# Performance work log

Measured on AMD Instinct MI355X. Metric: run time of the kernel, lower is better.

Reference implementation:

```python
import jax, jax.numpy as jnp
import numpy as np
from jax import lax

SPIKE_RATE = 100.0
TIME_STEPS = 100
ADAPT_FACTOR = 0.95
REFRACTORY = 2.0
N_NEURONS = 256


def setup_inputs() -> dict:
    key = jax.random.key(0)
    x = jax.random.normal(jax.random.fold_in(key, 1), (32, 64), dtype=jnp.float32)
    centers = jnp.linspace(-1.0, 1.0, N_NEURONS).astype(jnp.float32)
    widths = jnp.full((N_NEURONS,), 0.2, dtype=jnp.float32)
    adaptation_state = jnp.ones((N_NEURONS,), dtype=jnp.float32)
    refractory_state = jnp.zeros((N_NEURONS,), dtype=jnp.float32)
    return {
        "x": x,
        "centers": centers,
        "widths": widths,
        "adaptation_state": adaptation_state,
        "refractory_state": refractory_state,
        "seed": 0,
    }


def reference(x, centers, widths, adaptation_state, refractory_state, seed):
    # x: [B, F]; centers/widths/states: [N]
    # Gaussian tuning-curve response: [B, F, N]
    d = x[:, :, None] - centers[None, None, :]
    response = jnp.exp(-(d * d) / (2.0 * widths * widths))
    # adaptation applied once with the initial buffer state (as in torch source)
    response = response * adaptation_state[None, None, :]
    spike_prob = response * (SPIKE_RATE / 1000.0)

    base_key = jax.random.key(seed)

    def step(carry, t):
        ref, adapt = carry  # each [N]
        k = jax.random.fold_in(base_key, t)
        r = jax.random.uniform(k, spike_prob.shape, dtype=spike_prob.dtype)
        can_spike = (ref == 0).astype(spike_prob.dtype)  # [N]
        spike_t = (r < spike_prob).astype(spike_prob.dtype) * can_spike[None, None, :]
        ref = jnp.maximum(ref - 1.0, 0.0)
        occurred = spike_t.sum(axis=(0, 1)) > 0  # [N]
        ref = ref + occurred.astype(ref.dtype) * REFRACTORY
        adapt = adapt * jnp.where(occurred, ADAPT_FACTOR, 1.0)
        return (ref, adapt), spike_t

    (_, _), spikes = lax.scan(step, (refractory_state, adaptation_state),
                              jnp.arange(TIME_STEPS))
    # spikes: [T, B, F, N] -> [B, F, N, T] to match torch.stack(..., dim=-1)
    return jnp.moveaxis(spikes, 0, -1)
```

## Files before the change

### kernel.cpp

```cpp
#include <hip/hip_runtime.h>
#include <stdint.h>

typedef unsigned long long u64;
typedef unsigned int u32;

#define T_STEPS 100
#define NNEUR 256
#define NBF 2048
#define NELEM (NBF * NNEUR)
#define BF_PER_BLOCK 64
#define CHUNKS (NBF / BF_PER_BLOCK)

__device__ __forceinline__ void tf2x32(u32 k0, u32 k1, u32& x0, u32& x1) {
  u32 k2 = k0 ^ k1 ^ 0x1BD11BDAu;
  x0 += k0; x1 += k1;
#define TFR(r) { x0 += x1; x1 = (x1 << (r)) | (x1 >> (32 - (r))); x1 ^= x0; }
  TFR(13) TFR(15) TFR(26) TFR(6)
  x0 += k1; x1 += k2 + 1u;
  TFR(17) TFR(29) TFR(16) TFR(24)
  x0 += k2; x1 += k0 + 2u;
  TFR(13) TFR(15) TFR(26) TFR(6)
  x0 += k0; x1 += k1 + 3u;
  TFR(17) TFR(29) TFR(16) TFR(24)
  x0 += k1; x1 += k2 + 4u;
  TFR(13) TFR(15) TFR(26) TFR(6)
  x0 += k2; x1 += k0 + 5u;
#undef TFR
}

__global__ void __launch_bounds__(256) kern_p(
    const float* __restrict__ x, const float* __restrict__ c,
    const float* __restrict__ w, const float* __restrict__ a,
    float* __restrict__ p) {
  int idx = blockIdx.x * 256 + threadIdx.x;
  int n = idx & 255, bf = idx >> 8;
  float d = x[bf] - c[n];
  float denom = (2.0f * w[n]) * w[n];
  float q = -(d * d) / denom;
  float e = (float)exp((double)q);
  p[idx] = (e * a[n]) * 0.1f;
}

template <bool USE_P>
__global__ void __launch_bounds__(256) kern_bits(
    const float* __restrict__ p,
    const float* __restrict__ x, const float* __restrict__ c,
    const float* __restrict__ w, const float* __restrict__ a,
    const int* __restrict__ seedp,
    u64* __restrict__ cmp64,
    float* __restrict__ outf,
    u64* __restrict__ occ64) {
  const int t = blockIdx.x;
  const int chunk = blockIdx.y;
  const int lane = threadIdx.x & 63;
  const int v = threadIdx.x >> 6;
  const int n = v * 64 + lane;
  const u32 seed = (u32)seedp[0];

  u32 kt0 = 0u, kt1 = (u32)t;
  tf2x32(0u, seed, kt0, kt1);

  float cn = 0.f, wn = 0.f, an = 0.f;
  if (!USE_P) { cn = c[n]; wn = w[n]; an = a[n]; }

  bool occ = false;
#pragma unroll 2
  for (int j = 0; j < BF_PER_BLOCK; ++j) {
    int bf = chunk * BF_PER_BLOCK + j;
    u32 i = (u32)(bf * 256 + n);
    u32 b0 = 0u, b1 = i;
    tf2x32(kt0, kt1, b0, b1);
    u32 bits = b0 ^ b1;
    float r = __uint_as_float((bits >> 9) | 0x3F800000u) - 1.0f;
    float pv;
    if (USE_P) {
      pv = p[i];
    } else {
      float d = x[bf] - cn;
      float denom = (2.0f * wn) * wn;
      float q = -(d * d) / denom;
      pv = ((float)exp((double)q) * an) * 0.1f;
    }
    bool cm = r < pv;
    occ |= cm;
    if (USE_P) {
      u64 m = __ballot(cm);
      if (lane == 0) cmp64[((u64)bf * T_STEPS + (u64)t) * 4 + v] = m;
    } else {
      outf[(u64)bf * (NNEUR * T_STEPS) + (u64)n * T_STEPS + t] = cm ? 1.0f : 0.0f;
    }
  }
  u64 om = __ballot(occ);
  if (lane == 0) atomicOr(&occ64[t * 4 + v], om);
}

__global__ void __launch_bounds__(256) kern_rec(
    const float* __restrict__ ref0,
    const u64* __restrict__ occ64,
    u64* __restrict__ can64) {
  int n = threadIdx.x;
  int lane = n & 63, v = n >> 6;
  float ref = ref0[n];
  for (int t = 0; t < T_STEPS; ++t) {
    bool can = (ref == 0.0f);
    u64 cm = __ballot(can);
    if (lane == 0) can64[t * 4 + v] = cm;
    bool occb = (occ64[t * 4 + v] >> lane) & 1ull;
    bool occurred = can && occb;
    ref = fmaxf(ref - 1.0f, 0.0f) + (occurred ? 2.0f : 0.0f);
  }
}

__global__ void __launch_bounds__(256) kern_out(
    const u32* __restrict__ cmp32,
    const u32* __restrict__ can32,
    float* __restrict__ out) {
  __shared__ u32 s[T_STEPS * 8];
  const int bf = blockIdx.x;
  const int tid = threadIdx.x;
  for (int l = tid; l < T_STEPS * 8; l += 256) {
    int t = l >> 3, ww = l & 7;
    s[l] = cmp32[((u64)bf * T_STEPS + (u64)t) * 8 + ww] & can32[t * 8 + ww];
  }
  __syncthreads();
  float4* outv = (float4*)(out + (u64)bf * (NNEUR * T_STEPS));
#pragma unroll
  for (int k = 0; k < 25; ++k) {
    int q = tid + 256 * k;
    int e = q * 4;
    float4 val;
    float* vp = (float*)&val;
#pragma unroll
    for (int j = 0; j < 4; ++j) {
      int ee = e + j;
      int n = ee / 100;
      int t = ee - n * 100;
      vp[j] = (float)((s[t * 8 + (n >> 5)] >> (n & 31)) & 1u);
    }
    outv[q] = val;
  }
}

__global__ void __launch_bounds__(256) kern_mask(
    const u32* __restrict__ can32, float* __restrict__ out) {
  u64 q = (u64)blockIdx.x * 256 + threadIdx.x;
  float4* ov = (float4*)out;
  float4 vx = ov[q];
  u32 local = (u32)((q * 4) % (NNEUR * T_STEPS));
  float* vp = (float*)&vx;
#pragma unroll
  for (int j = 0; j < 4; ++j) {
    u32 le = local + j;
    u32 n = le / 100;
    u32 t = le - n * 100;
    u32 bit = (can32[t * 8 + (n >> 5)] >> (n & 31)) & 1u;
    vp[j] = bit ? vp[j] : 0.0f;
  }
  ov[q] = vx;
}

extern "C" void kernel_launch(void* const* d_in, const int* in_sizes, int n_in,
                              void* d_out, int out_size, void* d_ws, size_t ws_size,
                              hipStream_t stream) {
  const float* x  = (const float*)d_in[0];
  const float* c  = (const float*)d_in[1];
  const float* w  = (const float*)d_in[2];
  const float* a  = (const float*)d_in[3];
  const float* r0 = (const float*)d_in[4];
  const int* seed = (const int*)d_in[5];
  float* out = (float*)d_out;

  const size_t P_BYTES   = (size_t)NELEM * 4;
  const size_t CMP_BYTES = (size_t)NBF * T_STEPS * 4 * 8;
  const size_t OCC_BYTES = (size_t)T_STEPS * 4 * 8;
  const size_t CAN_BYTES = OCC_BYTES;
  const bool full = ws_size >= P_BYTES + CMP_BYTES + OCC_BYTES + CAN_BYTES;

  uint8_t* wsb = (uint8_t*)d_ws;
  float* p = nullptr; u64* cmp = nullptr; u64* occ; u64* can;
  if (full) {
    p   = (float*)wsb;
    cmp = (u64*)(wsb + P_BYTES);
    occ = (u64*)(wsb + P_BYTES + CMP_BYTES);
    can = (u64*)(wsb + P_BYTES + CMP_BYTES + OCC_BYTES);
  } else {
    occ = (u64*)wsb;
    can = (u64*)(wsb + OCC_BYTES);
  }

  hipMemsetAsync(occ, 0, OCC_BYTES, stream);

  if (full) {
    kern_p<<<NELEM / 256, 256, 0, stream>>>(x, c, w, a, p);
    kern_bits<true><<<dim3(T_STEPS, CHUNKS), 256, 0, stream>>>(
        p, x, c, w, a, seed, cmp, out, occ);
    kern_rec<<<1, 256, 0, stream>>>(r0, occ, can);
    kern_out<<<NBF, 256, 0, stream>>>((const u32*)cmp, (const u32*)can, out);
  } else {
    kern_bits<false><<<dim3(T_STEPS, CHUNKS), 256, 0, stream>>>(
        nullptr, x, c, w, a, seed, nullptr, out, occ);
    kern_rec<<<1, 256, 0, stream>>>(r0, occ, can);
    kern_mask<<<(out_size / 4) / 256, 256, 0, stream>>>((const u32*)can, out);
  }
}
```

Measured before the change: 415.2 us.

## Pack spike bits per thread with integer thresholds and fuse recurrence into output kernel

The probability array becomes integer thresholds (ceil of p*2^23), so the comparison is done on raw mantissa bits without a float conversion. The bits kernel now has each thread produce one 32-bit word covering 32 consecutive neurons, with the threefry key schedule hoisted and rotates done via alignbit. It combines words with shuffles and fewer atomics, where it previously used a per-element ballot. The serial refractory recurrence moves into every output block, removing a single-block launch at the cost of redundant work per block. The integer threshold must match float `r < p` exactly, which is a correctness risk at boundary values.

```diff
diff --git a/kernel.cpp b/kernel.cpp
--- a/kernel.cpp
+++ b/kernel.cpp
@@ -8,8 +8,6 @@
 #define NNEUR 256
 #define NBF 2048
 #define NELEM (NBF * NNEUR)
-#define BF_PER_BLOCK 64
-#define CHUNKS (NBF / BF_PER_BLOCK)
 
 __device__ __forceinline__ void tf2x32(u32 k0, u32 k1, u32& x0, u32& x1) {
   u32 k2 = k0 ^ k1 ^ 0x1BD11BDAu;
@@ -28,26 +26,153 @@
 #undef TFR
 }
 
+__device__ __forceinline__ u32 rotl32(u32 x, int r) {
+  return __builtin_amdgcn_alignbit(x, x, 32 - r);
+}
+
 __global__ void __launch_bounds__(256) kern_p(
     const float* __restrict__ x, const float* __restrict__ c,
     const float* __restrict__ w, const float* __restrict__ a,
-    float* __restrict__ p) {
+    u32* __restrict__ thr) {
   int idx = blockIdx.x * 256 + threadIdx.x;
   int n = idx & 255, bf = idx >> 8;
   float d = x[bf] - c[n];
   float denom = (2.0f * w[n]) * w[n];
   float q = -(d * d) / denom;
   float e = (float)exp((double)q);
-  p[idx] = (e * a[n]) * 0.1f;
-}
-
-template <bool USE_P>
-__global__ void __launch_bounds__(256) kern_bits(
-    const float* __restrict__ p,
+  float p = (e * a[n]) * 0.1f;
+  thr[idx] = (u32)ceilf(p * 8388608.0f);
+}
+
+__global__ void __launch_bounds__(256, 8) kern_bits2(
+    const u32* __restrict__ thr,
+    const int* __restrict__ seedp,
+    u32* __restrict__ cmp32,
+    u32* __restrict__ occ32) {
+  const int t = blockIdx.x;
+  const int g = blockIdx.y;
+  const int tid = threadIdx.x;
+  const int oct = tid & 7;
+  const int bfl = tid >> 3;
+  const int bf = g * 32 + bfl;
+  const u32 seed = (u32)seedp[0];
+
+  u32 K0 = 0u, K1 = (u32)t;
+  tf2x32(0u, seed, K0, K1);
+  const u32 K2 = K0 ^ K1 ^ 0x1BD11BDAu;
+  const u32 I01 = K1 + 1u + K2;
+  const u32 I10 = K1;
+  const u32 I11 = K2 + 1u;
+  const u32 I20 = K2;
+  const u32 I21 = K0 + 2u;
+  const u32 I30 = K0;
+  const u32 I31 = K1 + 3u;
+  const u32 I40 = K1;
+  const u32 I41 = K2 + 4u;
+  const u32 I50 = K2;
+  const u32 I51 = K0 + 5u;
+  (void)I01;
+
+  const u32 base_i = (u32)(bf * 256 + oct * 32);
+
+  u32 th[32];
+  const uint4* tp = (const uint4*)(thr + base_i);
+#pragma unroll
+  for (int q = 0; q < 8; ++q) {
+    uint4 v = tp[q];
+    th[4*q] = v.x; th[4*q+1] = v.y; th[4*q+2] = v.z; th[4*q+3] = v.w;
+  }
+
+  const u32 x1base = base_i + K1;
+  u32 word = 0u;
+#pragma unroll
+  for (int k = 31; k >= 0; --k) {
+    u32 x0 = K0;
+    u32 x1 = x1base + (u32)k;
+#define QR(r) { x0 += x1; x1 = rotl32(x1, r); x1 ^= x0; }
+    QR(13) QR(15) QR(26) QR(6)
+    x0 += I10; x1 += I11;
+    QR(17) QR(29) QR(16) QR(24)
+    x0 += I20; x1 += I21;
+    QR(13) QR(15) QR(26) QR(6)
+    x0 += I30; x1 += I31;
+    QR(17) QR(29) QR(16) QR(24)
+    x0 += I40; x1 += I41;
+    QR(13) QR(15) QR(26) QR(6)
+    x0 += I50; x1 += I51;
+#undef QR
+    u32 m = (x0 ^ x1) >> 9;
+    word = (word << 1) | (m < th[k] ? 1u : 0u);
+  }
+
+  cmp32[((u32)bf * T_STEPS + (u32)t) * 8 + oct] = word;
+
+  u32 o = word;
+  o |= (u32)__shfl_xor((int)o, 8, 64);
+  o |= (u32)__shfl_xor((int)o, 16, 64);
+  o |= (u32)__shfl_xor((int)o, 32, 64);
+  if ((tid & 63) < 8) atomicOr(&occ32[t * 8 + oct], o);
+}
+
+__global__ void __launch_bounds__(256) kern_out2(
+    const u32* __restrict__ cmp32,
+    const u32* __restrict__ occ32,
+    const float* __restrict__ ref0,
+    float* __restrict__ out) {
+  __shared__ u32 s_occ[T_STEPS * 8];
+  __shared__ u32 s_can[T_STEPS * 8];
+  __shared__ u32 s[T_STEPS * 8];
+  const int bf = blockIdx.x;
+  const int tid = threadIdx.x;
+
+  for (int l = tid; l < T_STEPS * 8; l += 256) s_occ[l] = occ32[l];
+  __syncthreads();
+
+  {
+    const int n = tid, lane = n & 63, v = n >> 6;
+    float ref = ref0[n];
+    for (int t = 0; t < T_STEPS; ++t) {
+      bool can = (ref == 0.0f);
+      u64 cm = __ballot(can);
+      if (lane == 0) {
+        s_can[t * 8 + v * 2]     = (u32)cm;
+        s_can[t * 8 + v * 2 + 1] = (u32)(cm >> 32);
+      }
+      bool occb = (s_occ[t * 8 + (n >> 5)] >> (n & 31)) & 1u;
+      bool occurred = can && occb;
+      ref = fmaxf(ref - 1.0f, 0.0f) + (occurred ? 2.0f : 0.0f);
+    }
+  }
+  __syncthreads();
+
+  for (int l = tid; l < T_STEPS * 8; l += 256) {
+    int t = l >> 3, ww = l & 7;
+    s[l] = cmp32[((u64)bf * T_STEPS + (u64)t) * 8 + ww] & s_can[l];
+  }
+  __syncthreads();
+
+  float4* outv = (float4*)(out + (u64)bf * (NNEUR * T_STEPS));
+#pragma unroll
+  for (int kk = 0; kk < 25; ++kk) {
+    int q = tid + 256 * kk;
+    int e = q * 4;
+    float4 val;
+    float* vp = (float*)&val;
+#pragma unroll
+    for (int j = 0; j < 4; ++j) {
+      int ee = e + j;
+      int n = ee / 100;
+      int t = ee - n * 100;
+      vp[j] = (float)((s[t * 8 + (n >> 5)] >> (n & 31)) & 1u);
+    }
+    outv[q] = val;
+  }
+}
+
+__global__ void __launch_bounds__(256) kern_bits_fb(
     const float* __restrict__ x, const float* __restrict__ c,
     const float* __restrict__ w, const float* __restrict__ a,
     const int* __restrict__ seedp,
-    u64* __restrict__ cmp64,
     float* __restrict__ outf,
     u64* __restrict__ occ64) {
   const int t = blockIdx.x;
@@ -56,39 +181,24 @@
   const int v = threadIdx.x >> 6;
   const int n = v * 64 + lane;
   const u32 seed = (u32)seedp[0];
-
   u32 kt0 = 0u, kt1 = (u32)t;
   tf2x32(0u, seed, kt0, kt1);
-
-  float cn = 0.f, wn = 0.f, an = 0.f;
-  if (!USE_P) { cn = c[n]; wn = w[n]; an = a[n]; }
-
+  float cn = c[n], wn = w[n], an = a[n];
   bool occ = false;
-#pragma unroll 2
-  for (int j = 0; j < BF_PER_BLOCK; ++j) {
-    int bf = chunk * BF_PER_BLOCK + j;
+  for (int j = 0; j < 64; ++j) {
+    int bf = chunk * 64 + j;
     u32 i = (u32)(bf * 256 + n);
     u32 b0 = 0u, b1 = i;
     tf2x32(kt0, kt1, b0, b1);
     u32 bits = b0 ^ b1;
     float r = __uint_as_float((bits >> 9) | 0x3F800000u) - 1.0f;
-    float pv;
-    if (USE_P) {
-      pv = p[i];
-    } else {
-      float d = x[bf] - cn;
-      float denom = (2.0f * wn) * wn;
-      float q = -(d * d) / denom;
-      pv = ((float)exp((double)q) * an) * 0.1f;
-    }
+    float d = x[bf] - cn;
+    float denom = (2.0f * wn) * wn;
+    float q = -(d * d) / denom;
+    float pv = ((float)exp((double)q) * an) * 0.1f;
     bool cm = r < pv;
     occ |= cm;
-    if (USE_P) {
-      u64 m = __ballot(cm);
-      if (lane == 0) cmp64[((u64)bf * T_STEPS + (u64)t) * 4 + v] = m;
-    } else {
-      outf[(u64)bf * (NNEUR * T_STEPS) + (u64)n * T_STEPS + t] = cm ? 1.0f : 0.0f;
-    }
+    outf[(u64)bf * (NNEUR * T_STEPS) + (u64)n * T_STEPS + t] = cm ? 1.0f : 0.0f;
   }
   u64 om = __ballot(occ);
   if (lane == 0) atomicOr(&occ64[t * 4 + v], om);
@@ -111,36 +221,6 @@
   }
 }
 
-__global__ void __launch_bounds__(256) kern_out(
-    const u32* __restrict__ cmp32,
-    const u32* __restrict__ can32,
-    float* __restrict__ out) {
-  __shared__ u32 s[T_STEPS * 8];
-  const int bf = blockIdx.x;
-  const int tid = threadIdx.x;
-  for (int l = tid; l < T_STEPS * 8; l += 256) {
-    int t = l >> 3, ww = l & 7;
-    s[l] = cmp32[((u64)bf * T_STEPS + (u64)t) * 8 + ww] & can32[t * 8 + ww];
-  }
-  __syncthreads();
-  float4* outv = (float4*)(out + (u64)bf * (NNEUR * T_STEPS));
-#pragma unroll
-  for (int k = 0; k < 25; ++k) {
-    int q = tid + 256 * k;
-    int e = q * 4;
-    float4 val;
-    float* vp = (float*)&val;
-#pragma unroll
-    for (int j = 0; j < 4; ++j) {
-      int ee = e + j;
-      int n = ee / 100;
-      int t = ee - n * 100;
-      vp[j] = (float)((s[t * 8 + (n >> 5)] >> (n & 31)) & 1u);
-    }
-    outv[q] = val;
-  }
-}
-
 __global__ void __launch_bounds__(256) kern_mask(
     const u32* __restrict__ can32, float* __restrict__ out) {
   u64 q = (u64)blockIdx.x * 256 + threadIdx.x;
@@ -173,32 +253,23 @@
   const size_t P_BYTES   = (size_t)NELEM * 4;
   const size_t CMP_BYTES = (size_t)NBF * T_STEPS * 4 * 8;
   const size_t OCC_BYTES = (size_t)T_STEPS * 4 * 8;
-  const size_t CAN_BYTES = OCC_BYTES;
-  const bool full = ws_size >= P_BYTES + CMP_BYTES + OCC_BYTES + CAN_BYTES;
+  const bool full = ws_size >= P_BYTES + CMP_BYTES + 2 * OCC_BYTES;
 
   uint8_t* wsb = (uint8_t*)d_ws;
-  float* p = nullptr; u64* cmp = nullptr; u64* occ; u64* can;
+
   if (full) {
-    p   = (float*)wsb;
-    cmp = (u64*)(wsb + P_BYTES);
-    occ = (u64*)(wsb + P_BYTES + CMP_BYTES);
-    can = (u64*)(wsb + P_BYTES + CMP_BYTES + OCC_BYTES);
+    u32* thr   = (u32*)wsb;
+    u32* cmp   = (u32*)(wsb + P_BYTES);
+    u32* occ   = (u32*)(wsb + P_BYTES + CMP_BYTES);
+    hipMemsetAsync(occ, 0, OCC_BYTES, stream);
+    kern_p<<<NELEM / 256, 256, 0, stream>>>(x, c, w, a, thr);
+    kern_bits2<<<dim3(T_STEPS, 64), 256, 0, stream>>>(thr, seed, cmp, occ);
+    kern_out2<<<NBF, 256, 0, stream>>>(cmp, occ, r0, out);
   } else {
-    occ = (u64*)wsb;
-    can = (u64*)(wsb + OCC_BYTES);
-  }
-
-  hipMemsetAsync(occ, 0, OCC_BYTES, stream);
-
-  if (full) {
-    kern_p<<<NELEM / 256, 256, 0, stream>>>(x, c, w, a, p);
-    kern_bits<true><<<dim3(T_STEPS, CHUNKS), 256, 0, stream>>>(
-        p, x, c, w, a, seed, cmp, out, occ);
-    kern_rec<<<1, 256, 0, stream>>>(r0, occ, can);
-    kern_out<<<NBF, 256, 0, stream>>>((const u32*)cmp, (const u32*)can, out);
-  } else {
-    kern_bits<false><<<dim3(T_STEPS, CHUNKS), 256, 0, stream>>>(
-        nullptr, x, c, w, a, seed, nullptr, out, occ);
+    u64* occ = (u64*)wsb;
+    u64* can = (u64*)(wsb + OCC_BYTES);
+    hipMemsetAsync(occ, 0, OCC_BYTES, stream);
+    kern_bits_fb<<<dim3(T_STEPS, 32), 256, 0, stream>>>(x, c, w, a, seed, out, occ);
     kern_rec<<<1, 256, 0, stream>>>(r0, occ, can);
     kern_mask<<<(out_size / 4) / 256, 256, 0, stream>>>((const u32*)can, out);
   }
```

After: 363.6 us. 1.14x faster.
